# Kernel optimization log

Measured on AMD Instinct MI355X. Metric: run time of the kernel, lower is better.

Reference implementation:

```python
import jax, jax.numpy as jnp
import numpy as np
import math

EMBED_DIM = 1024
BATCH = 4
SEQ = 2048


def setup_inputs() -> dict:
    key = jax.random.key(0)
    ks = jax.random.split(key, 7)
    d = EMBED_DIM
    s = 1.0 / math.sqrt(d)
    x = jax.random.normal(ks[0], (BATCH, SEQ, d), dtype=jnp.float32)
    Wq = jax.random.normal(ks[1], (d, d), dtype=jnp.float32) * s
    Wk = jax.random.normal(ks[2], (d, d), dtype=jnp.float32) * s
    Wv = jax.random.normal(ks[3], (d, d), dtype=jnp.float32) * s
    bq = jax.random.normal(ks[4], (d,), dtype=jnp.float32) * 0.01
    bk = jax.random.normal(ks[5], (d,), dtype=jnp.float32) * 0.01
    bv = jax.random.normal(ks[6], (d,), dtype=jnp.float32) * 0.01
    return {"x": x, "Wq": Wq, "bq": bq, "Wk": Wk, "bk": bk, "Wv": Wv, "bv": bv}


def reference(x, Wq, bq, Wk, bk, Wv, bv):
    # q/k/v: [B, S, D] linear projections (weights stored as [in, out])
    q = jnp.einsum('bsd,de->bse', x, Wq) + bq
    k = jnp.einsum('bsd,de->bse', x, Wk) + bk
    v = jnp.einsum('bsd,de->bse', x, Wv) + bv
    scale = jnp.sqrt(jnp.asarray(x.shape[-1], dtype=x.dtype))
    # full O(S^2) score matrix, as in the original (non-fused) attention
    attn_scores = jnp.einsum('bqd,bkd->bqk', q, k) / scale
    attn_probs = jax.nn.softmax(attn_scores, axis=-1)
    # lxa.strassen(attn_probs, v) is a (Strassen) matmul: same math as matmul
    return jnp.einsum('bqk,bkd->bqd', attn_probs, v)
```

## Files before the change

### kernel.cpp

```cpp
#include <hip/hip_runtime.h>
#include <stdint.h>

#define SEQ 2048
#define DIM 1024
#define NB 4
#define MTOT (NB*SEQ)
#define QKVN (3*DIM)

typedef __attribute__((ext_vector_type(8))) short short8;
typedef __attribute__((ext_vector_type(4))) float f32x4;

__device__ __forceinline__ unsigned short f2b(float f) {
    union { float f; unsigned int u; } v; v.f = f;
    return (unsigned short)((v.u + 0x7FFFu + ((v.u >> 16) & 1u)) >> 16);
}

__device__ __forceinline__ void gload_lds16(const unsigned short* g, unsigned short* l) {
    __builtin_amdgcn_global_load_lds(
        (const __attribute__((address_space(1))) void*)g,
        (__attribute__((address_space(3))) void*)l, 16, 0, 0);
}

__device__ __forceinline__ short8 ds128(unsigned addr) {
    short8 r;
    asm volatile("ds_read_b128 %0, %1" : "=v"(r) : "v"(addr));
    return r;
}

#define FENCE_BARRIER do { asm volatile("" ::: "memory"); \
    __builtin_amdgcn_s_barrier(); asm volatile("" ::: "memory"); } while (0)

__device__ __forceinline__ int xcd_swz(int bid, int nwg) {
    if (nwg & 7) return bid;
    return (bid & 7) * (nwg >> 3) + (bid >> 3);
}


__global__ __launch_bounds__(256)
void cast_kernel(const float* __restrict__ in, unsigned short* __restrict__ out, int nchunk) {
    int i = blockIdx.x * 256 + threadIdx.x;
    if (i >= nchunk) return;
    float4 a = ((const float4*)in)[i*2];
    float4 b = ((const float4*)in)[i*2+1];
    union { unsigned short u[8]; uint4 v; } r;
    r.u[0]=f2b(a.x); r.u[1]=f2b(a.y); r.u[2]=f2b(a.z); r.u[3]=f2b(a.w);
    r.u[4]=f2b(b.x); r.u[5]=f2b(b.y); r.u[6]=f2b(b.z); r.u[7]=f2b(b.w);
    ((uint4*)out)[i] = r.v;
}

__global__ __launch_bounds__(256)
void transpose_cast_f32(const float* __restrict__ in, unsigned short* __restrict__ out, int R, int C) {
    __shared__ unsigned short tile[64][66];
    int tpc = C >> 6;
    int tr = (blockIdx.x / tpc) << 6;
    int tc = (blockIdx.x % tpc) << 6;
    int t = threadIdx.x;
    #pragma unroll
    for (int i = 0; i < 16; i++) {
        int idx = t + i*256;
        int r = idx >> 6, c = idx & 63;
        tile[r][c] = f2b(in[(size_t)(tr + r)*C + tc + c]);
    }
    __syncthreads();
    #pragma unroll
    for (int i = 0; i < 16; i++) {
        int idx = t + i*256;
        int r = idx >> 6, c = idx & 63;
        out[(size_t)(tc + r)*R + tr + c] = tile[c][r];
    }
}

__global__ __launch_bounds__(256)
void transpose_b16(const unsigned short* __restrict__ in0, size_t sIn, int ldin,
                   unsigned short* __restrict__ out0, size_t sOut, int ldout, int tpc) {
    const unsigned short* in = in0 + sIn * blockIdx.y;
    unsigned short* out = out0 + sOut * blockIdx.y;
    __shared__ unsigned short tile[64][66];
    int tr = ((int)blockIdx.x / tpc) << 6;
    int tc = ((int)blockIdx.x % tpc) << 6;
    int t = threadIdx.x;
    #pragma unroll
    for (int i = 0; i < 16; i++) {
        int idx = t + i*256;
        int r = idx >> 6, c = idx & 63;
        tile[r][c] = in[(size_t)(tr + r)*ldin + tc + c];
    }
    __syncthreads();
    #pragma unroll
    for (int i = 0; i < 16; i++) {
        int idx = t + i*256;
        int r = idx >> 6, c = idx & 63;
        out[(size_t)(tc + r)*ldout + tr + c] = tile[c][r];
    }
}

__global__ __launch_bounds__(256)
void bias_concat(const float* __restrict__ bq, const float* __restrict__ bk,
                 const float* __restrict__ bv, float* __restrict__ o) {
    int i = blockIdx.x*256 + threadIdx.x;
    float v = (i < DIM) ? bq[i] : ((i < 2*DIM) ? bk[i-DIM] : bv[i-2*DIM]);
    o[i] = v;
}


__device__ __forceinline__ void stage1(const unsigned short* __restrict__ Xb, int ldx,
                                       unsigned short* dstBase, int h, int k0,
                                       int tid, int wid) {
    int srow = tid >> 3;
    int scol = ((tid & 7) ^ (srow & 7)) << 3;
    const unsigned short* g = Xb + (size_t)(h*128 + srow)*ldx + k0 + scol;
    unsigned short* d = dstBase + h*8192 + wid*512;
    gload_lds16(g, d);
    gload_lds16(g + (size_t)64*ldx, d + 4096);
}

#define RD_A(BUF, QM) do { _Pragma("unroll") for (int mf = 0; mf < 4; ++mf) { \
    fa[mf][0] = ds128(As0 + (BUF)*32768u + (QM)*16384u + aRow + mf*2048u + c0); \
    fa[mf][1] = ds128(As0 + (BUF)*32768u + (QM)*16384u + aRow + mf*2048u + c1); } } while (0)

#define RD_B(BUF, QN) do { _Pragma("unroll") for (int nf = 0; nf < 2; ++nf) { \
    fb[nf][0] = ds128(Bs0 + (BUF)*32768u + (QN)*16384u + bRow + nf*2048u + c0); \
    fb[nf][1] = ds128(Bs0 + (BUF)*32768u + (QN)*16384u + bRow + nf*2048u + c1); } } while (0)

#define MMA_PH(QM, QN) do { \
    asm volatile("s_waitcnt lgkmcnt(0)" ::: "memory"); \
    __builtin_amdgcn_sched_barrier(0); \
    __builtin_amdgcn_s_setprio(1); \
    _Pragma("unroll") for (int mf = 0; mf < 4; ++mf) \
      _Pragma("unroll") for (int nf = 0; nf < 2; ++nf) \
        _Pragma("unroll") for (int ks = 0; ks < 2; ++ks) \
          acc[QM][QN][mf][nf] = __builtin_amdgcn_mfma_f32_16x16x32_bf16( \
              fa[mf][ks], fb[nf][ks], acc[QM][QN][mf][nf], 0, 0, 0); \
    __builtin_amdgcn_s_setprio(0); \
} while (0)

template<int MODE>
__global__ __launch_bounds__(512, 2)
void gemm8p(const unsigned short* __restrict__ A, int lda, size_t sA,
            const unsigned short* __restrict__ Bt, int ldb, size_t sB,
            const float* __restrict__ bias,
            void* __restrict__ Cout, int ldc, size_t sC,
            int N, int K)
{
    __shared__ __align__(16) unsigned short As[2][16384];
    __shared__ __align__(16) unsigned short Bs[2][16384];
    int nbn = N >> 8;
    int bid = xcd_swz((int)blockIdx.x, (int)gridDim.x);
    int bm = bid / nbn, bn = bid % nbn;
    int bz = blockIdx.y;
    int tid = threadIdx.x;
    int lane = tid & 63;
    int wid  = tid >> 6;
    int wm = (wid >> 2) & 1;
    int wn = wid & 3;
    int rlo = lane & 15;
    int shi = lane >> 4;

    unsigned As0 = (unsigned)(uintptr_t)&As[0][0];
    unsigned Bs0 = (unsigned)(uintptr_t)&Bs[0][0];
    unsigned c0 = (unsigned)(((shi     ^ rlo) & 7) * 16);
    unsigned c1 = (unsigned)((((4+shi) ^ rlo) & 7) * 16);
    unsigned aRow = (unsigned)((wm*64 + rlo) * 128);
    unsigned bRow = (unsigned)((wn*32 + rlo) * 128);

    f32x4 acc[2][2][4][2];
    #pragma unroll
    for (int a = 0; a < 2; a++)
        #pragma unroll
        for (int b = 0; b < 2; b++)
            #pragma unroll
            for (int c = 0; c < 4; c++)
                #pragma unroll
                for (int d = 0; d < 2; d++)
                    acc[a][b][c][d] = (f32x4){0.f,0.f,0.f,0.f};

    const unsigned short* Ab = A + sA*bz + (size_t)(bm*256)*lda;
    const unsigned short* Bb = Bt + sB*bz + (size_t)(bn*256)*ldb;

    stage1(Ab, lda, &As[0][0], 0, 0,  tid, wid);
    stage1(Bb, ldb, &Bs[0][0], 0, 0,  tid, wid);
    stage1(Ab, lda, &As[0][0], 1, 0,  tid, wid);
    stage1(Bb, ldb, &Bs[0][0], 1, 0,  tid, wid);
    stage1(Ab, lda, &As[1][0], 0, 64, tid, wid);
    stage1(Bb, ldb, &Bs[1][0], 1, 64, tid, wid);
    stage1(Ab, lda, &As[1][0], 1, 64, tid, wid);
    __builtin_amdgcn_sched_barrier(0);
    asm volatile("s_waitcnt vmcnt(6)" ::: "memory");
    FENCE_BARRIER;

    short8 fa[4][2], fb[2][2];
    int nt = K >> 6;
    int nit = nt >> 1;

    for (int it = 0; it < nit; ++it) {
        int kO  = (2*it + 1) << 6;
        int kE2 = (2*it + 2 < nt) ? (2*it + 2) << 6 : 0;
        int kO2 = (2*it + 3 < nt) ? (2*it + 3) << 6 : 0;

        RD_A(0, 0); RD_B(0, 0);
        stage1(Bb, ldb, &Bs[1][0], 0, kO, tid, wid);
        asm volatile("s_waitcnt lgkmcnt(8)" ::: "memory");
        FENCE_BARRIER; MMA_PH(0, 0); FENCE_BARRIER;
        RD_B(0, 1);
        stage1(Ab, lda, &As[0][0], 0, kE2, tid, wid);
        FENCE_BARRIER; MMA_PH(0, 1); FENCE_BARRIER;
        RD_A(0, 1);
        stage1(Bb, ldb, &Bs[0][0], 1, kE2, tid, wid);
        FENCE_BARRIER; MMA_PH(1, 1); FENCE_BARRIER;
        RD_B(0, 0);
        stage1(Ab, lda, &As[0][0], 1, kE2, tid, wid);
        __builtin_amdgcn_sched_barrier(0);
        asm volatile("s_waitcnt vmcnt(6)" ::: "memory");
        FENCE_BARRIER; MMA_PH(1, 0); FENCE_BARRIER;
        RD_A(1, 0); RD_B(1, 0);
        stage1(Bb, ldb, &Bs[0][0], 0, kE2, tid, wid);
        asm volatile("s_waitcnt lgkmcnt(8)" ::: "memory");
        FENCE_BARRIER; MMA_PH(0, 0); FENCE_BARRIER;
        RD_B(1, 1);
        stage1(Ab, lda, &As[1][0], 0, kO2, tid, wid);
        FENCE_BARRIER; MMA_PH(0, 1); FENCE_BARRIER;
        RD_A(1, 1);
        stage1(Bb, ldb, &Bs[1][0], 1, kO2, tid, wid);
        FENCE_BARRIER; MMA_PH(1, 1); FENCE_BARRIER;
        RD_B(1, 0);
        stage1(Ab, lda, &As[1][0], 1, kO2, tid, wid);
        __builtin_amdgcn_sched_barrier(0);
        asm volatile("s_waitcnt vmcnt(6)" ::: "memory");
        FENCE_BARRIER; MMA_PH(1, 0); FENCE_BARRIER;
    }

    asm volatile("s_waitcnt vmcnt(0)" ::: "memory");

    int r0 = shi << 2;
    unsigned short* Cu = (unsigned short*)Cout + sC*bz;
    float* Cf = (float*)Cout + sC*bz;
    #pragma unroll
    for (int qm = 0; qm < 2; ++qm)
        #pragma unroll
        for (int qn = 0; qn < 2; ++qn)
            #pragma unroll
            for (int mf = 0; mf < 4; ++mf)
                #pragma unroll
                for (int nf = 0; nf < 2; ++nf) {
                    int col = bn*256 + qn*128 + wn*32 + nf*16 + rlo;
                    float badd = (MODE == 0) ? bias[col] : 0.f;
                    #pragma unroll
                    for (int r = 0; r < 4; ++r) {
                        int row = bm*256 + qm*128 + wm*64 + mf*16 + r0 + r;
                        float v = acc[qm][qn][mf][nf][r];
                        if (MODE == 0) Cu[(size_t)row*ldc + col] = f2b(v + badd);
                        else           Cf[(size_t)row*ldc + col] = v;
                    }
                }
}

__global__ __launch_bounds__(256, 2)
void gemm_nt_pv(const unsigned short* __restrict__ A, int lda, size_t sA,
                const unsigned short* __restrict__ Bt, int ldb, size_t sB,
                float* __restrict__ Cout, int ldc, size_t sC,
                int N, int K)
{
    __shared__ __align__(16) unsigned short As[128][64];
    __shared__ __align__(16) unsigned short Bs[128][64];
    int nbn = N >> 7;
    int bid = xcd_swz((int)blockIdx.x, (int)gridDim.x);
    int bm = bid / nbn;
    int bn = bid % nbn;
    int bz = blockIdx.y;
    int tid = threadIdx.x;
    int lane = tid & 63;
    int wid  = tid >> 6;
    int wm = (wid >> 1) * 64, wn = (wid & 1) * 64;
    int lr = lane & 15;
    int lk = (lane >> 4) * 8;
    int srow = lane >> 3;
    int scol = (lane & 7) * 8;

    f32x4 acc[4][4];
    #pragma unroll
    for (int i = 0; i < 4; i++)
        #pragma unroll
        for (int j = 0; j < 4; j++) acc[i][j] = (f32x4){0.f,0.f,0.f,0.f};

    const unsigned short* Ab = A + sA*bz + (size_t)(bm*128)*lda;
    const unsigned short* Bb = Bt + sB*bz + (size_t)(bn*128)*ldb;

    for (int k0 = 0; k0 < K; k0 += 64) {
        #pragma unroll
        for (int r = 0; r < 4; r++) {
            int rowg = r*32 + wid*8;
            gload_lds16(Ab + (size_t)(rowg + srow)*lda + k0 + scol, &As[rowg][0]);
            gload_lds16(Bb + (size_t)(rowg + srow)*ldb + k0 + scol, &Bs[rowg][0]);
        }
        __syncthreads();
        #pragma unroll
        for (int ks = 0; ks < 2; ks++) {
            short8 af[4], bfr[4];
            #pragma unroll
            for (int mf = 0; mf < 4; mf++)
                af[mf] = *(const short8*)&As[wm + mf*16 + lr][ks*32 + lk];
            #pragma unroll
            for (int nf = 0; nf < 4; nf++)
                bfr[nf] = *(const short8*)&Bs[wn + nf*16 + lr][ks*32 + lk];
            #pragma unroll
            for (int mf = 0; mf < 4; mf++)
                #pragma unroll
                for (int nf = 0; nf < 4; nf++)
                    acc[mf][nf] = __builtin_amdgcn_mfma_f32_16x16x32_bf16(af[mf], bfr[nf], acc[mf][nf], 0, 0, 0);
        }
        __syncthreads();
    }

    int r0 = (lane >> 4) << 2;
    float* Cf = Cout + sC*bz;
    #pragma unroll
    for (int mf = 0; mf < 4; mf++)
        #pragma unroll
        for (int nf = 0; nf < 4; nf++) {
            int col = bn*128 + wn + nf*16 + lr;
            #pragma unroll
            for (int r = 0; r < 4; r++) {
                int row = bm*128 + wm + mf*16 + r0 + r;
                Cf[(size_t)row*ldc + col] = acc[mf][nf][r];
            }
        }
}

__global__ __launch_bounds__(256)
void softmax_kernel(float* __restrict__ S, float scl) {
    int row = blockIdx.x;
    float* srow = S + (size_t)row * SEQ;
    int t = threadIdx.x;
    float4 v0 = ((const float4*)srow)[t*2];
    float4 v1 = ((const float4*)srow)[t*2+1];
    float x[8] = {v0.x*scl,v0.y*scl,v0.z*scl,v0.w*scl,v1.x*scl,v1.y*scl,v1.z*scl,v1.w*scl};
    float m = fmaxf(fmaxf(fmaxf(x[0],x[1]),fmaxf(x[2],x[3])),
                    fmaxf(fmaxf(x[4],x[5]),fmaxf(x[6],x[7])));
    #pragma unroll
    for (int off = 32; off; off >>= 1) m = fmaxf(m, __shfl_xor(m, off));
    __shared__ float redm[4], reds[4];
    int w = t >> 6;
    if ((t & 63) == 0) redm[w] = m;
    __syncthreads();
    m = fmaxf(fmaxf(redm[0], redm[1]), fmaxf(redm[2], redm[3]));
    float e[8]; float s = 0.f;
    #pragma unroll
    for (int i = 0; i < 8; i++) { e[i] = __expf(x[i] - m); s += e[i]; }
    #pragma unroll
    for (int off = 32; off; off >>= 1) s += __shfl_xor(s, off);
    if ((t & 63) == 0) reds[w] = s;
    __syncthreads();
    float inv = 1.0f / (reds[0]+reds[1]+reds[2]+reds[3]);
    union { unsigned short u[8]; uint4 v; } r;
    #pragma unroll
    for (int i = 0; i < 8; i++) r.u[i] = f2b(e[i] * inv);
    ((uint4*)srow)[t] = r.v;
}

extern "C" void kernel_launch(void* const* d_in, const int* in_sizes, int n_in,
                              void* d_out, int out_size, void* d_ws, size_t ws_size,
                              hipStream_t stream)
{
    (void)in_sizes; (void)n_in; (void)out_size;
    const float* x  = (const float*)d_in[0];
    const float* Wq = (const float*)d_in[1];
    const float* bq = (const float*)d_in[2];
    const float* Wk = (const float*)d_in[3];
    const float* bk = (const float*)d_in[4];
    const float* Wv = (const float*)d_in[5];
    const float* bv = (const float*)d_in[6];
    float* out = (float*)d_out;

    unsigned short* qkv = (unsigned short*)d_ws;
    unsigned short* vt  = qkv + (size_t)MTOT*QKVN;
    float* biasc = (float*)(vt + (size_t)NB*DIM*SEQ);
    char* ovl = (char*)biasc + 65536;
    unsigned short* xb    = (unsigned short*)ovl;
    unsigned short* wqkvt = xb + (size_t)MTOT*DIM;
    float* scores = (float*)ovl;

    size_t base = (size_t)MTOT*QKVN*2 + (size_t)NB*DIM*SEQ*2 + 65536;
    int bpp = 1;
    if (base + 4*(size_t)SEQ*SEQ*4 <= ws_size) bpp = 4;
    else if (base + 2*(size_t)SEQ*SEQ*4 <= ws_size) bpp = 2;

    cast_kernel<<<MTOT*DIM/8/256, 256, 0, stream>>>(x, xb, MTOT*DIM/8);
    transpose_cast_f32<<<256, 256, 0, stream>>>(Wq, wqkvt,             DIM, DIM);
    transpose_cast_f32<<<256, 256, 0, stream>>>(Wk, wqkvt + DIM*DIM,   DIM, DIM);
    transpose_cast_f32<<<256, 256, 0, stream>>>(Wv, wqkvt + 2*DIM*DIM, DIM, DIM);
    bias_concat<<<QKVN/256, 256, 0, stream>>>(bq, bk, bv, biasc);

    gemm8p<0><<<dim3((MTOT/256)*(QKVN/256)), 512, 0, stream>>>(
        xb, DIM, 0, wqkvt, DIM, 0, biasc, qkv, QKVN, 0, QKVN, DIM);

    transpose_b16<<<dim3((SEQ/64)*(DIM/64), NB), 256, 0, stream>>>(
        qkv + 2*DIM, (size_t)SEQ*QKVN, QKVN, vt, (size_t)DIM*SEQ, SEQ, DIM/64);

    const float scl = 1.0f / 32.0f;
    for (int p = 0; p < NB; p += bpp) {
        const unsigned short* qp = qkv + (size_t)p*SEQ*QKVN;
        gemm8p<1><<<dim3((SEQ/256)*(SEQ/256), bpp), 512, 0, stream>>>(
            qp,       QKVN, (size_t)SEQ*QKVN,
            qp + DIM, QKVN, (size_t)SEQ*QKVN,
            nullptr, scores, SEQ, (size_t)SEQ*SEQ, SEQ, DIM);
        softmax_kernel<<<bpp*SEQ, 256, 0, stream>>>(scores, scl);
        gemm_nt_pv<<<dim3((SEQ/128)*(DIM/128), bpp), 256, 0, stream>>>(
            (const unsigned short*)scores, 2*SEQ, (size_t)SEQ*2*SEQ,
            vt + (size_t)p*DIM*SEQ,        SEQ,   (size_t)DIM*SEQ,
            out + (size_t)p*SEQ*DIM, DIM, (size_t)SEQ*DIM, DIM, SEQ);
    }
}
```

Before: 192.9 us.

## Shrink GEMM tile to 128x256 and reuse it for the PV product

Replaces the 256x256 eight-phase GEMM with a 128x256 four-phase variant that halves the A tile and accumulator registers, doubling the grid size for the QKV and score GEMMs. The separate simple PV GEMM kernel is removed and the PV product now runs through the same pipelined LDS-direct kernel with 512 threads. The aim is better CU occupancy and wave count plus a better-pipelined PV matmul. The cost is lower data reuse per tile, which raises global and LDS traffic per FLOP.

```diff
diff --git a/kernel.cpp b/kernel.cpp
--- a/kernel.cpp
+++ b/kernel.cpp
@@ -114,35 +114,35 @@
     gload_lds16(g + (size_t)64*ldx, d + 4096);
 }
 
-#define RD_A(BUF, QM) do { _Pragma("unroll") for (int mf = 0; mf < 4; ++mf) { \
-    fa[mf][0] = ds128(As0 + (BUF)*32768u + (QM)*16384u + aRow + mf*2048u + c0); \
-    fa[mf][1] = ds128(As0 + (BUF)*32768u + (QM)*16384u + aRow + mf*2048u + c1); } } while (0)
+#define RD_A(BUF) do { _Pragma("unroll") for (int mf = 0; mf < 4; ++mf) { \
+    fa[mf][0] = ds128(As0 + (BUF)*16384u + aRow + mf*2048u + c0); \
+    fa[mf][1] = ds128(As0 + (BUF)*16384u + aRow + mf*2048u + c1); } } while (0)
 
 #define RD_B(BUF, QN) do { _Pragma("unroll") for (int nf = 0; nf < 2; ++nf) { \
     fb[nf][0] = ds128(Bs0 + (BUF)*32768u + (QN)*16384u + bRow + nf*2048u + c0); \
     fb[nf][1] = ds128(Bs0 + (BUF)*32768u + (QN)*16384u + bRow + nf*2048u + c1); } } while (0)
 
-#define MMA_PH(QM, QN) do { \
+#define MMA_PH(QN) do { \
     asm volatile("s_waitcnt lgkmcnt(0)" ::: "memory"); \
     __builtin_amdgcn_sched_barrier(0); \
     __builtin_amdgcn_s_setprio(1); \
     _Pragma("unroll") for (int mf = 0; mf < 4; ++mf) \
       _Pragma("unroll") for (int nf = 0; nf < 2; ++nf) \
         _Pragma("unroll") for (int ks = 0; ks < 2; ++ks) \
-          acc[QM][QN][mf][nf] = __builtin_amdgcn_mfma_f32_16x16x32_bf16( \
-              fa[mf][ks], fb[nf][ks], acc[QM][QN][mf][nf], 0, 0, 0); \
+          acc[QN][mf][nf] = __builtin_amdgcn_mfma_f32_16x16x32_bf16( \
+              fa[mf][ks], fb[nf][ks], acc[QN][mf][nf], 0, 0, 0); \
     __builtin_amdgcn_s_setprio(0); \
 } while (0)
 
 template<int MODE>
 __global__ __launch_bounds__(512, 2)
-void gemm8p(const unsigned short* __restrict__ A, int lda, size_t sA,
+void gemm4p(const unsigned short* __restrict__ A, int lda, size_t sA,
             const unsigned short* __restrict__ Bt, int ldb, size_t sB,
             const float* __restrict__ bias,
             void* __restrict__ Cout, int ldc, size_t sC,
             int N, int K)
 {
-    __shared__ __align__(16) unsigned short As[2][16384];
+    __shared__ __align__(16) unsigned short As[2][8192];
     __shared__ __align__(16) unsigned short Bs[2][16384];
     int nbn = N >> 8;
     int bid = xcd_swz((int)blockIdx.x, (int)gridDim.x);
@@ -163,29 +163,25 @@
     unsigned aRow = (unsigned)((wm*64 + rlo) * 128);
     unsigned bRow = (unsigned)((wn*32 + rlo) * 128);
 
-    f32x4 acc[2][2][4][2];
+    f32x4 acc[2][4][2];
     #pragma unroll
     for (int a = 0; a < 2; a++)
         #pragma unroll
-        for (int b = 0; b < 2; b++)
+        for (int b = 0; b < 4; b++)
             #pragma unroll
-            for (int c = 0; c < 4; c++)
-                #pragma unroll
-                for (int d = 0; d < 2; d++)
-                    acc[a][b][c][d] = (f32x4){0.f,0.f,0.f,0.f};
-
-    const unsigned short* Ab = A + sA*bz + (size_t)(bm*256)*lda;
+            for (int c = 0; c < 2; c++)
+                acc[a][b][c] = (f32x4){0.f,0.f,0.f,0.f};
+
+    const unsigned short* Ab = A + sA*bz + (size_t)(bm*128)*lda;
     const unsigned short* Bb = Bt + sB*bz + (size_t)(bn*256)*ldb;
 
     stage1(Ab, lda, &As[0][0], 0, 0,  tid, wid);
     stage1(Bb, ldb, &Bs[0][0], 0, 0,  tid, wid);
-    stage1(Ab, lda, &As[0][0], 1, 0,  tid, wid);
     stage1(Bb, ldb, &Bs[0][0], 1, 0,  tid, wid);
     stage1(Ab, lda, &As[1][0], 0, 64, tid, wid);
-    stage1(Bb, ldb, &Bs[1][0], 1, 64, tid, wid);
-    stage1(Ab, lda, &As[1][0], 1, 64, tid, wid);
+    stage1(Bb, ldb, &Bs[1][0], 0, 64, tid, wid);
     __builtin_amdgcn_sched_barrier(0);
-    asm volatile("s_waitcnt vmcnt(6)" ::: "memory");
+    asm volatile("s_waitcnt vmcnt(4)" ::: "memory");
     FENCE_BARRIER;
 
     short8 fa[4][2], fb[2][2];
@@ -197,36 +193,26 @@
         int kE2 = (2*it + 2 < nt) ? (2*it + 2) << 6 : 0;
         int kO2 = (2*it + 3 < nt) ? (2*it + 3) << 6 : 0;
 
-        RD_A(0, 0); RD_B(0, 0);
-        stage1(Bb, ldb, &Bs[1][0], 0, kO, tid, wid);
+        RD_A(0); RD_B(0, 0);
+        stage1(Bb, ldb, &Bs[1][0], 1, kO, tid, wid);
         asm volatile("s_waitcnt lgkmcnt(8)" ::: "memory");
-        FENCE_BARRIER; MMA_PH(0, 0); FENCE_BARRIER;
+        FENCE_BARRIER; MMA_PH(0); FENCE_BARRIER;
         RD_B(0, 1);
         stage1(Ab, lda, &As[0][0], 0, kE2, tid, wid);
-        FENCE_BARRIER; MMA_PH(0, 1); FENCE_BARRIER;
-        RD_A(0, 1);
+        stage1(Bb, ldb, &Bs[0][0], 0, kE2, tid, wid);
+        __builtin_amdgcn_sched_barrier(0);
+        asm volatile("s_waitcnt vmcnt(4)" ::: "memory");
+        FENCE_BARRIER; MMA_PH(1); FENCE_BARRIER;
+        RD_A(1); RD_B(1, 0);
         stage1(Bb, ldb, &Bs[0][0], 1, kE2, tid, wid);
-        FENCE_BARRIER; MMA_PH(1, 1); FENCE_BARRIER;
-        RD_B(0, 0);
-        stage1(Ab, lda, &As[0][0], 1, kE2, tid, wid);
-        __builtin_amdgcn_sched_barrier(0);
-        asm volatile("s_waitcnt vmcnt(6)" ::: "memory");
-        FENCE_BARRIER; MMA_PH(1, 0); FENCE_BARRIER;
-        RD_A(1, 0); RD_B(1, 0);
-        stage1(Bb, ldb, &Bs[0][0], 0, kE2, tid, wid);
         asm volatile("s_waitcnt lgkmcnt(8)" ::: "memory");
-        FENCE_BARRIER; MMA_PH(0, 0); FENCE_BARRIER;
+        FENCE_BARRIER; MMA_PH(0); FENCE_BARRIER;
         RD_B(1, 1);
         stage1(Ab, lda, &As[1][0], 0, kO2, tid, wid);
-        FENCE_BARRIER; MMA_PH(0, 1); FENCE_BARRIER;
-        RD_A(1, 1);
-        stage1(Bb, ldb, &Bs[1][0], 1, kO2, tid, wid);
-        FENCE_BARRIER; MMA_PH(1, 1); FENCE_BARRIER;
-        RD_B(1, 0);
-        stage1(Ab, lda, &As[1][0], 1, kO2, tid, wid);
+        stage1(Bb, ldb, &Bs[1][0], 0, kO2, tid, wid);
         __builtin_amdgcn_sched_barrier(0);
-        asm volatile("s_waitcnt vmcnt(6)" ::: "memory");
-        FENCE_BARRIER; MMA_PH(1, 0); FENCE_BARRIER;
+        asm volatile("s_waitcnt vmcnt(4)" ::: "memory");
+        FENCE_BARRIER; MMA_PH(1); FENCE_BARRIER;
     }
 
     asm volatile("s_waitcnt vmcnt(0)" ::: "memory");
@@ -235,95 +221,21 @@
     unsigned short* Cu = (unsigned short*)Cout + sC*bz;
     float* Cf = (float*)Cout + sC*bz;
     #pragma unroll
-    for (int qm = 0; qm < 2; ++qm)
+    for (int qn = 0; qn < 2; ++qn)
         #pragma unroll
-        for (int qn = 0; qn < 2; ++qn)
+        for (int mf = 0; mf < 4; ++mf)
             #pragma unroll
-            for (int mf = 0; mf < 4; ++mf)
+            for (int nf = 0; nf < 2; ++nf) {
+                int col = bn*256 + qn*128 + wn*32 + nf*16 + rlo;
+                float badd = (MODE == 0) ? bias[col] : 0.f;
                 #pragma unroll
-                for (int nf = 0; nf < 2; ++nf) {
-                    int col = bn*256 + qn*128 + wn*32 + nf*16 + rlo;
-                    float badd = (MODE == 0) ? bias[col] : 0.f;
-                    #pragma unroll
-                    for (int r = 0; r < 4; ++r) {
-                        int row = bm*256 + qm*128 + wm*64 + mf*16 + r0 + r;
-                        float v = acc[qm][qn][mf][nf][r];
-                        if (MODE == 0) Cu[(size_t)row*ldc + col] = f2b(v + badd);
-                        else           Cf[(size_t)row*ldc + col] = v;
-                    }
+                for (int r = 0; r < 4; ++r) {
+                    int row = bm*128 + wm*64 + mf*16 + r0 + r;
+                    float v = acc[qn][mf][nf][r];
+                    if (MODE == 0) Cu[(size_t)row*ldc + col] = f2b(v + badd);
+                    else           Cf[(size_t)row*ldc + col] = v;
                 }
-}
-
-__global__ __launch_bounds__(256, 2)
-void gemm_nt_pv(const unsigned short* __restrict__ A, int lda, size_t sA,
-                const unsigned short* __restrict__ Bt, int ldb, size_t sB,
-                float* __restrict__ Cout, int ldc, size_t sC,
-                int N, int K)
-{
-    __shared__ __align__(16) unsigned short As[128][64];
-    __shared__ __align__(16) unsigned short Bs[128][64];
-    int nbn = N >> 7;
-    int bid = xcd_swz((int)blockIdx.x, (int)gridDim.x);
-    int bm = bid / nbn;
-    int bn = bid % nbn;
-    int bz = blockIdx.y;
-    int tid = threadIdx.x;
-    int lane = tid & 63;
-    int wid  = tid >> 6;
-    int wm = (wid >> 1) * 64, wn = (wid & 1) * 64;
-    int lr = lane & 15;
-    int lk = (lane >> 4) * 8;
-    int srow = lane >> 3;
-    int scol = (lane & 7) * 8;
-
-    f32x4 acc[4][4];
-    #pragma unroll
-    for (int i = 0; i < 4; i++)
-        #pragma unroll
-        for (int j = 0; j < 4; j++) acc[i][j] = (f32x4){0.f,0.f,0.f,0.f};
-
-    const unsigned short* Ab = A + sA*bz + (size_t)(bm*128)*lda;
-    const unsigned short* Bb = Bt + sB*bz + (size_t)(bn*128)*ldb;
-
-    for (int k0 = 0; k0 < K; k0 += 64) {
-        #pragma unroll
-        for (int r = 0; r < 4; r++) {
-            int rowg = r*32 + wid*8;
-            gload_lds16(Ab + (size_t)(rowg + srow)*lda + k0 + scol, &As[rowg][0]);
-            gload_lds16(Bb + (size_t)(rowg + srow)*ldb + k0 + scol, &Bs[rowg][0]);
-        }
-        __syncthreads();
-        #pragma unroll
-        for (int ks = 0; ks < 2; ks++) {
-            short8 af[4], bfr[4];
-            #pragma unroll
-            for (int mf = 0; mf < 4; mf++)
-                af[mf] = *(const short8*)&As[wm + mf*16 + lr][ks*32 + lk];
-            #pragma unroll
-            for (int nf = 0; nf < 4; nf++)
-                bfr[nf] = *(const short8*)&Bs[wn + nf*16 + lr][ks*32 + lk];
-            #pragma unroll
-            for (int mf = 0; mf < 4; mf++)
-                #pragma unroll
-                for (int nf = 0; nf < 4; nf++)
-                    acc[mf][nf] = __builtin_amdgcn_mfma_f32_16x16x32_bf16(af[mf], bfr[nf], acc[mf][nf], 0, 0, 0);
-        }
-        __syncthreads();
-    }
-
-    int r0 = (lane >> 4) << 2;
-    float* Cf = Cout + sC*bz;
-    #pragma unroll
-    for (int mf = 0; mf < 4; mf++)
-        #pragma unroll
-        for (int nf = 0; nf < 4; nf++) {
-            int col = bn*128 + wn + nf*16 + lr;
-            #pragma unroll
-            for (int r = 0; r < 4; r++) {
-                int row = bm*128 + wm + mf*16 + r0 + r;
-                Cf[(size_t)row*ldc + col] = acc[mf][nf][r];
             }
-        }
 }
 
 __global__ __launch_bounds__(256)
@@ -390,7 +302,7 @@
     transpose_cast_f32<<<256, 256, 0, stream>>>(Wv, wqkvt + 2*DIM*DIM, DIM, DIM);
     bias_concat<<<QKVN/256, 256, 0, stream>>>(bq, bk, bv, biasc);
 
-    gemm8p<0><<<dim3((MTOT/256)*(QKVN/256)), 512, 0, stream>>>(
+    gemm4p<0><<<dim3((MTOT/128)*(QKVN/256)), 512, 0, stream>>>(
         xb, DIM, 0, wqkvt, DIM, 0, biasc, qkv, QKVN, 0, QKVN, DIM);
 
     transpose_b16<<<dim3((SEQ/64)*(DIM/64), NB), 256, 0, stream>>>(
@@ -399,14 +311,14 @@
     const float scl = 1.0f / 32.0f;
     for (int p = 0; p < NB; p += bpp) {
         const unsigned short* qp = qkv + (size_t)p*SEQ*QKVN;
-        gemm8p<1><<<dim3((SEQ/256)*(SEQ/256), bpp), 512, 0, stream>>>(
+        gemm4p<1><<<dim3((SEQ/128)*(SEQ/256), bpp), 512, 0, stream>>>(
             qp,       QKVN, (size_t)SEQ*QKVN,
             qp + DIM, QKVN, (size_t)SEQ*QKVN,
             nullptr, scores, SEQ, (size_t)SEQ*SEQ, SEQ, DIM);
         softmax_kernel<<<bpp*SEQ, 256, 0, stream>>>(scores, scl);
-        gemm_nt_pv<<<dim3((SEQ/128)*(DIM/128), bpp), 256, 0, stream>>>(
+        gemm4p<1><<<dim3((SEQ/128)*(DIM/256), bpp), 512, 0, stream>>>(
             (const unsigned short*)scores, 2*SEQ, (size_t)SEQ*2*SEQ,
             vt + (size_t)p*DIM*SEQ,        SEQ,   (size_t)DIM*SEQ,
-            out + (size_t)p*SEQ*DIM, DIM, (size_t)SEQ*DIM, DIM, SEQ);
-    }
-}
+            nullptr, out + (size_t)p*SEQ*DIM, DIM, (size_t)SEQ*DIM, DIM, SEQ);
+    }
+}
```

After: 189.4 us, median of 2. Within noise of the previous version (-1.8%).
